# Performance work log

Measured on AMD Instinct MI355X. Metric: run time of the kernel, lower is better.

Reference implementation:

```python
import jax, jax.numpy as jnp
import numpy as np

D_MODEL = 1024
N_HEADS = 16
D_K = D_MODEL // N_HEADS
NEG = -1e10


def setup_inputs() -> dict:
    key = jax.random.key(0)
    ks = jax.random.split(key, 12)
    bs, sl = 2, 2048
    q = jax.random.normal(ks[0], (bs, sl, D_MODEL), dtype=jnp.float32)
    k = jax.random.normal(ks[1], (bs, sl, D_MODEL), dtype=jnp.float32)
    v = jax.random.normal(ks[2], (bs, sl, D_MODEL), dtype=jnp.float32)
    mask = jax.random.randint(ks[3], (bs, 1, sl, sl), 0, 2).astype(bool)
    s = 1.0 / np.sqrt(D_MODEL)
    Wq = jax.random.uniform(ks[4], (D_MODEL, D_MODEL), jnp.float32, -s, s)
    bq = jax.random.uniform(ks[5], (D_MODEL,), jnp.float32, -s, s)
    Wk = jax.random.uniform(ks[6], (D_MODEL, D_MODEL), jnp.float32, -s, s)
    bk = jax.random.uniform(ks[7], (D_MODEL,), jnp.float32, -s, s)
    Wv = jax.random.uniform(ks[8], (D_MODEL, D_MODEL), jnp.float32, -s, s)
    bv = jax.random.uniform(ks[9], (D_MODEL,), jnp.float32, -s, s)
    Wo = jax.random.uniform(ks[10], (D_MODEL, D_MODEL), jnp.float32, -s, s)
    bo = jax.random.uniform(ks[11], (D_MODEL,), jnp.float32, -s, s)
    return {"q": q, "k": k, "v": v, "mask": mask,
            "Wq": Wq, "bq": bq, "Wk": Wk, "bk": bk,
            "Wv": Wv, "bv": bv, "Wo": Wo, "bo": bo}


def reference(q, k, v, mask, Wq, bq, Wk, bk, Wv, bv, Wo, bo):
    bs, sl, _ = q.shape
    sl2 = k.shape[1]
    # linear projections (torch Linear: x @ W.T + b), split into heads: [b, h, s, d_k]
    qh = (q @ Wq.T + bq).reshape(bs, sl, N_HEADS, D_K).transpose(0, 2, 1, 3)
    kh = (k @ Wk.T + bk).reshape(bs, sl2, N_HEADS, D_K).transpose(0, 2, 1, 3)
    vh = (v @ Wv.T + bv).reshape(bs, sl2, N_HEADS, D_K).transpose(0, 2, 1, 3)
    scores = jnp.einsum('bhqd,bhkd->bhqk', qh, kh) / jnp.sqrt(jnp.float32(D_K))
    scores = jnp.where(mask, NEG, scores)
    attn = jax.nn.softmax(scores, axis=-1)
    z = jnp.einsum('bhqk,bhkd->bhqd', attn, vh)  # [b, h, sl, d_k]
    z = z.transpose(0, 2, 1, 3).reshape(bs, sl, D_MODEL)
    return z @ Wo.T + bo
```

## Files before the change

### kernel.cpp

```cpp
#include <hip/hip_runtime.h>

typedef __attribute__((ext_vector_type(8))) short short8;
typedef __attribute__((ext_vector_type(4))) float f32x4;
typedef __attribute__((ext_vector_type(16))) float f32x16;
typedef __attribute__((ext_vector_type(4))) unsigned int u32x4;

#define MFMA16(a, b, c) __builtin_amdgcn_mfma_f32_16x16x32_bf16((a), (b), (c), 0, 0, 0)
#define MFMA32(a, b, c) __builtin_amdgcn_mfma_f32_32x32x16_bf16((a), (b), (c), 0, 0, 0)

#if __has_builtin(__builtin_amdgcn_exp2f)
#define EXP2(x) __builtin_amdgcn_exp2f(x)
#else
#define EXP2(x) __expf((x) * 0.6931471805599453f)
#endif

__device__ __forceinline__ unsigned short f2bf(float f) {
  unsigned int u = __float_as_uint(f);
  u += 0x7FFFu + ((u >> 16) & 1u);
  return (unsigned short)(u >> 16);
}

__device__ __forceinline__ unsigned int cvtpk(float lo, float hi) {
  unsigned int r;
  asm("v_cvt_pk_bf16_f32 %0, %1, %2" : "=v"(r) : "v"(lo), "v"(hi));
  return r;
}

__device__ __forceinline__ short8 mk8(unsigned int a, unsigned int b,
                                      unsigned int c, unsigned int d) {
  u32x4 u = {a, b, c, d};
  return __builtin_bit_cast(short8, u);
}

__device__ __forceinline__ void gload16(const void* g, void* l) {
  __builtin_amdgcn_global_load_lds((const __attribute__((address_space(1))) void*)g,
                                   (__attribute__((address_space(3))) void*)l, 16, 0, 0);
}

__device__ __forceinline__ int swz(int row) {
  return (row & 7) ^ (((row >> 3) & 3) << 1);
}

__device__ __forceinline__ short8 fragld64(const unsigned short* base, int row, int kchunk) {
  int cc = kchunk ^ swz(row);
  return *(const short8*)(base + row * 64 + cc * 8);
}

__global__ void cvt3(const float* __restrict__ a, const float* __restrict__ b,
                     const float* __restrict__ c, unsigned short* __restrict__ out, int n4) {
  const float* src = (blockIdx.z == 0) ? a : ((blockIdx.z == 1) ? b : c);
  int i = blockIdx.x * blockDim.x + threadIdx.x;
  if (i >= n4) return;
  float4 v = ((const float4*)src)[i];
  ushort4 o;
  o.x = f2bf(v.x); o.y = f2bf(v.y); o.z = f2bf(v.z); o.w = f2bf(v.w);
  ((ushort4*)(out + (size_t)blockIdx.z * (size_t)n4 * 4))[i] = o;
}

__global__ void cvt4(const float* __restrict__ a, const float* __restrict__ b,
                     const float* __restrict__ c, const float* __restrict__ d,
                     unsigned short* __restrict__ out, int n4) {
  const float* src = (blockIdx.z == 0) ? a : ((blockIdx.z == 1) ? b
                   : ((blockIdx.z == 2) ? c : d));
  int i = blockIdx.x * blockDim.x + threadIdx.x;
  if (i >= n4) return;
  float4 v = ((const float4*)src)[i];
  ushort4 o;
  o.x = f2bf(v.x); o.y = f2bf(v.y); o.z = f2bf(v.z); o.w = f2bf(v.w);
  ((ushort4*)(out + (size_t)blockIdx.z * (size_t)n4 * 4))[i] = o;
}

__global__ void maskpack(const int* __restrict__ m, unsigned long long* __restrict__ mw) {
  const int lane = threadIdx.x & 63;
  const size_t wbase = ((size_t)blockIdx.x * (blockDim.x >> 6) + (threadIdx.x >> 6)) * 4ull;
#pragma unroll
  for (int u = 0; u < 4; ++u) {
    size_t word = wbase + u;
    int x = m[word * 64 + lane];
    unsigned long long bb = __ballot(x != 0);
    if (lane == 0) mw[word] = bb;
  }
}

__global__ void vtrans(const unsigned short* __restrict__ vh, unsigned short* __restrict__ vtg) {
  __shared__ unsigned short t[64][66];
  const int sx = blockIdx.x * 64, h = blockIdx.y, b = blockIdx.z;
  const int tid = threadIdx.x;
  const int r = tid >> 2, c0 = (tid & 3) * 16;
  const unsigned short* src = vh + ((size_t)(b * 2048 + sx + r)) * 1024 + h * 64 + c0;
  short8 x0 = *(const short8*)src;
  short8 x1 = *(const short8*)(src + 8);
#pragma unroll
  for (int e = 0; e < 8; ++e) {
    t[c0 + e][r] = (unsigned short)x0[e];
    t[c0 + 8 + e][r] = (unsigned short)x1[e];
  }
  __syncthreads();
  short8 y0, y1;
#pragma unroll
  for (int e = 0; e < 8; ++e) {
    y0[e] = (short)t[r][c0 + e];
    y1[e] = (short)t[r][c0 + 8 + e];
  }
  unsigned short* dst = vtg + ((size_t)((b * 16 + h) * 64 + r)) * 2048 + sx + c0;
  *(short8*)dst = y0;
  *(short8*)(dst + 8) = y1;
}

template<bool OUT_BF16>
__global__ __launch_bounds__(256, 3) void gemm_bt(
    const unsigned short* __restrict__ Abase, const unsigned short* __restrict__ Bbase,
    const float* __restrict__ bias0, const float* __restrict__ bias1,
    const float* __restrict__ bias2, void* __restrict__ outv, float scale0)
{
  constexpr int K = 1024, N = 1024;
  const int z = blockIdx.z;
  const unsigned short* A = Abase + (size_t)z * 4194304ull;
  const unsigned short* B = Bbase + (size_t)z * 1048576ull;
  const float* bias = (z == 0) ? bias0 : ((z == 1) ? bias1 : bias2);
  const float scale = (z == 0) ? scale0 : 1.0f;

  __shared__ unsigned short ldsA[128 * 64];
  __shared__ unsigned short ldsB[128 * 64];

  const int tid = threadIdx.x;
  const int lane = tid & 63, wid = tid >> 6;
  const int c16 = lane & 15, g = lane >> 4;
  const int m0 = blockIdx.y * 128, n0 = blockIdx.x * 128;
  const int wr = (wid >> 1) * 64, wc = (wid & 1) * 64;

  f32x4 acc[4][4] = {};

  for (int kt = 0; kt < K; kt += 64) {
    __syncthreads();
#pragma unroll
    for (int i = 0; i < 4; ++i) {
      int row = i * 32 + (tid >> 3);
      int cc = tid & 7;
      int scc = cc ^ swz(row);
      gload16(A + (size_t)(m0 + row) * K + kt + scc * 8, ldsA + row * 64 + cc * 8);
      gload16(B + (size_t)(n0 + row) * K + kt + scc * 8, ldsB + row * 64 + cc * 8);
    }
    __syncthreads();
#pragma unroll
    for (int kc = 0; kc < 2; ++kc) {
      short8 af[4], bf[4];
#pragma unroll
      for (int mi = 0; mi < 4; ++mi) af[mi] = fragld64(ldsA, wr + mi * 16 + c16, kc * 4 + g);
#pragma unroll
      for (int ni = 0; ni < 4; ++ni) bf[ni] = fragld64(ldsB, wc + ni * 16 + c16, kc * 4 + g);
#pragma unroll
      for (int mi = 0; mi < 4; ++mi)
#pragma unroll
        for (int ni = 0; ni < 4; ++ni)
          acc[mi][ni] = MFMA16(af[mi], bf[ni], acc[mi][ni]);
    }
  }

#pragma unroll
  for (int mi = 0; mi < 4; ++mi)
#pragma unroll
    for (int ni = 0; ni < 4; ++ni) {
      int col = n0 + wc + ni * 16 + c16;
      float bb = bias[col];
#pragma unroll
      for (int r = 0; r < 4; ++r) {
        int row = m0 + wr + mi * 16 + g * 4 + r;
        float v = (acc[mi][ni][r] + bb) * scale;
        if constexpr (OUT_BF16)
          ((unsigned short*)outv)[(size_t)z * 4194304ull + (size_t)row * N + col] = f2bf(v);
        else
          ((float*)outv)[(size_t)row * N + col] = v;
      }
    }
}

__device__ __forceinline__ void half_step(
    const unsigned short* __restrict__ kb, const unsigned short* __restrict__ vb,
    const short8 qf[4], unsigned int nb, int ql, int hd, int rowoff, int gm0,
    f32x16& z0, f32x16& z1, float& rs_out)
{
  f32x16 s;
#pragma unroll
  for (int m = 0; m < 4; ++m) {
    unsigned int nib = (nb >> (m * 8)) & 0xFu;
#pragma unroll
    for (int c = 0; c < 4; ++c)
      s[m * 4 + c] = ((nib >> c) & 1u) ? -1e10f : 0.0f;
  }
  __builtin_amdgcn_s_setprio(1);
#pragma unroll
  for (int kc = 0; kc < 4; ++kc)
    s = MFMA32(fragld64(kb, rowoff + ql, kc * 2 + hd), qf[kc], s);
  __builtin_amdgcn_s_setprio(0);
#pragma unroll
  for (int i = 0; i < 16; ++i) s[i] = EXP2(s[i]);
  {
    float a0 = (s[0] + s[1]) + (s[2] + s[3]);
    float a1 = (s[4] + s[5]) + (s[6] + s[7]);
    float a2 = (s[8] + s[9]) + (s[10] + s[11]);
    float a3 = (s[12] + s[13]) + (s[14] + s[15]);
    rs_out = (a0 + a1) + (a2 + a3);
  }
  unsigned int wv[8];
#pragma unroll
  for (int i = 0; i < 8; ++i) wv[i] = cvtpk(s[2 * i], s[2 * i + 1]);
  asm("v_permlane32_swap_b32 %0, %1" : "+v"(wv[0]), "+v"(wv[2]));
  asm("v_permlane32_swap_b32 %0, %1" : "+v"(wv[1]), "+v"(wv[3]));
  asm("v_permlane32_swap_b32 %0, %1" : "+v"(wv[4]), "+v"(wv[6]));
  asm("v_permlane32_swap_b32 %0, %1" : "+v"(wv[5]), "+v"(wv[7]));
  __builtin_amdgcn_s_setprio(1);
  {
    short8 pf0 = mk8(wv[0], wv[1], wv[2], wv[3]);
    z0 = MFMA32(pf0, fragld64(vb, ql, gm0 * 2 + hd), z0);
    z1 = MFMA32(pf0, fragld64(vb, 32 + ql, gm0 * 2 + hd), z1);
    short8 pf1 = mk8(wv[4], wv[5], wv[6], wv[7]);
    z0 = MFMA32(pf1, fragld64(vb, ql, (gm0 + 1) * 2 + hd), z0);
    z1 = MFMA32(pf1, fragld64(vb, 32 + ql, (gm0 + 1) * 2 + hd), z1);
  }
  __builtin_amdgcn_s_setprio(0);
}

__global__ __launch_bounds__(256, 3) void attn(
    const unsigned short* __restrict__ qh, const unsigned short* __restrict__ kh,
    const unsigned short* __restrict__ vtg, const unsigned long long* __restrict__ mw,
    unsigned short* __restrict__ zbf)
{
  constexpr int SL = 2048, DM = 1024, NT = SL / 64;
  const int bid = blockIdx.x;
  const int g = bid & 31;
  const int qt = bid >> 5;
  const int h = g & 15, b = g >> 4;

  const int tid = threadIdx.x, lane = tid & 63, w = tid >> 6;
  const int ql = lane & 31, hd = lane >> 5;
  const int qa = qt * 128 + w * 32;

  __shared__ unsigned short kbuf[2][4096];
  __shared__ unsigned short vbuf[2][4096];

  short8 qf[4];
  {
    const size_t qrow = ((size_t)b * SL + qa + ql) * DM + (size_t)h * 64 + hd * 8;
#pragma unroll
    for (int kc = 0; kc < 4; ++kc)
      qf[kc] = *(const short8*)(qh + qrow + kc * 16);
  }

  f32x16 zacc0 = {}, zacc1 = {};
  float lrun = 0.f;

  const unsigned long long* mwq = mw + ((size_t)b * SL + qa + ql) * (SL / 64);
  unsigned long long mwc = mwq[0];

  const int kr = tid >> 3, cc = tid & 7;
  const int r0 = kr, r1 = kr + 32;
  const size_t kbase = (size_t)b * SL * DM + (size_t)h * 64;
  const size_t vbase = (size_t)((b * 16 + h) * 64) * (size_t)SL;
  const unsigned short* kp0 = kh + kbase + (size_t)r0 * DM + (cc ^ swz(r0)) * 8;
  const unsigned short* kp1 = kh + kbase + (size_t)r1 * DM + (cc ^ swz(r1)) * 8;
  const unsigned short* vp0 = vtg + vbase + (size_t)r0 * SL + (cc ^ swz(r0)) * 8;
  const unsigned short* vp1 = vtg + vbase + (size_t)r1 * SL + (cc ^ swz(r1)) * 8;

  gload16(kp0, kbuf[0] + r0 * 64 + cc * 8);
  gload16(kp1, kbuf[0] + r1 * 64 + cc * 8);
  gload16(vp0, vbuf[0] + r0 * 64 + cc * 8);
  gload16(vp1, vbuf[0] + r1 * 64 + cc * 8);

  for (int t = 0; t < NT; ++t) {
    const int cur = t & 1, nxt = cur ^ 1;
    __syncthreads();

    const bool more = (t + 1 < NT);
    unsigned long long mwn = 0;
    if (more) {
      kp0 += 64 * DM; kp1 += 64 * DM; vp0 += 64; vp1 += 64;
      gload16(kp0, kbuf[nxt] + r0 * 64 + cc * 8);
      gload16(kp1, kbuf[nxt] + r1 * 64 + cc * 8);
      gload16(vp0, vbuf[nxt] + r0 * 64 + cc * 8);
      gload16(vp1, vbuf[nxt] + r1 * 64 + cc * 8);
      mwn = mwq[t + 1];
    }

    float rsA, rsB;
    half_step(kbuf[cur], vbuf[cur], qf, ((unsigned int)mwc) >> (hd * 4),
              ql, hd, 0, 0, zacc0, zacc1, rsA);
    half_step(kbuf[cur], vbuf[cur], qf, ((unsigned int)(mwc >> 32)) >> (hd * 4),
              ql, hd, 32, 2, zacc0, zacc1, rsB);
    lrun += rsA + rsB;
    mwc = mwn;
  }

  lrun += __shfl_xor(lrun, 32);

  float invl = (lrun > 0.f) ? 1.f / lrun : 0.f;
#pragma unroll
  for (int reg = 0; reg < 16; ++reg) {
    int qrow = (reg & 3) + 8 * (reg >> 2) + 4 * hd;
    float il = __shfl(invl, qrow);
    size_t orow = ((size_t)b * SL + qa + qrow) * DM + (size_t)h * 64;
    zbf[orow + ql] = f2bf(zacc0[reg] * il);
    zbf[orow + 32 + ql] = f2bf(zacc1[reg] * il);
  }
}

extern "C" void kernel_launch(void* const* d_in, const int* in_sizes, int n_in,
                              void* d_out, int out_size, void* d_ws, size_t ws_size,
                              hipStream_t stream) {
  const float* q  = (const float*)d_in[0];
  const float* k  = (const float*)d_in[1];
  const float* v  = (const float*)d_in[2];
  const int* mask = (const int*)d_in[3];
  const float* Wq = (const float*)d_in[4];
  const float* bq = (const float*)d_in[5];
  const float* Wk = (const float*)d_in[6];
  const float* bk = (const float*)d_in[7];
  const float* Wv = (const float*)d_in[8];
  const float* bv = (const float*)d_in[9];
  const float* Wo = (const float*)d_in[10];
  const float* bo = (const float*)d_in[11];

  char* ws = (char*)d_ws;
  unsigned short* xbf = (unsigned short*)ws;
  unsigned long long* mwb = (unsigned long long*)ws;
  unsigned short* zbf = (unsigned short*)(ws + 2097152);
  unsigned short* wbf = (unsigned short*)(ws + 25165824);
  unsigned short* qkv = (unsigned short*)(ws + 33554432);
  unsigned short* vtg = (unsigned short*)(ws + 58720256);

  cvt3<<<dim3(4096, 1, 3), 256, 0, stream>>>(q, k, v, xbf, 1048576);
  cvt4<<<dim3(1024, 1, 4), 256, 0, stream>>>(Wq, Wk, Wv, Wo, wbf, 262144);

  gemm_bt<true><<<dim3(8, 32, 3), 256, 0, stream>>>(xbf, wbf, bq, bk, bv, (void*)qkv,
                                                    0.125f * 1.44269504088896f);
  maskpack<<<8192, 256, 0, stream>>>(mask, mwb);
  vtrans<<<dim3(32, 16, 2), 256, 0, stream>>>(qkv + 8388608ull, vtg);
  attn<<<512, 256, 0, stream>>>(qkv, qkv + 4194304ull, vtg, mwb, zbf);
  gemm_bt<false><<<dim3(8, 32, 1), 256, 0, stream>>>(zbf, wbf + 3145728ull, bo, bo, bo, d_out, 1.0f);
}
```

Baseline: 148.0 us.

## Merge prep kernels and double attention K/V tile depth per barrier

The two fp32-to-bf16 conversion kernels become one launch, and the mask packing and V transpose kernels become another, cutting the launch count from seven to five. The attention loop now loads two 64-key tiles per stage, giving a 128-key stage, so there are half as many __syncthreads per row block and more loads in flight. LDS use per block doubles to 64KB, which may cut occupancy below the 3 blocks per CU set by launch bounds.

Result: no change. 147.1 us (-0.6%).

```diff
diff --git a/kernel.cpp b/kernel.cpp
--- a/kernel.cpp
+++ b/kernel.cpp
@@ -46,46 +46,50 @@
   return *(const short8*)(base + row * 64 + cc * 8);
 }
 
-__global__ void cvt3(const float* __restrict__ a, const float* __restrict__ b,
-                     const float* __restrict__ c, unsigned short* __restrict__ out, int n4) {
-  const float* src = (blockIdx.z == 0) ? a : ((blockIdx.z == 1) ? b : c);
-  int i = blockIdx.x * blockDim.x + threadIdx.x;
-  if (i >= n4) return;
-  float4 v = ((const float4*)src)[i];
+__global__ void prep(const float* __restrict__ q, const float* __restrict__ k,
+                     const float* __restrict__ v, const float* __restrict__ Wq,
+                     const float* __restrict__ Wk, const float* __restrict__ Wv,
+                     const float* __restrict__ Wo, unsigned short* __restrict__ xbf,
+                     unsigned short* __restrict__ wbf) {
+  const int bid = blockIdx.x, tid = threadIdx.x;
+  const float* src;
+  unsigned short* dst;
+  int i;
+  if (bid < 12288) {
+    int which = bid >> 12;
+    i = (bid & 4095) * 256 + tid;
+    src = (which == 0) ? q : ((which == 1) ? k : v);
+    dst = xbf + (size_t)which * 4194304ull;
+  } else {
+    int which = (bid - 12288) >> 10;
+    i = ((bid - 12288) & 1023) * 256 + tid;
+    src = (which == 0) ? Wq : ((which == 1) ? Wk : ((which == 2) ? Wv : Wo));
+    dst = wbf + (size_t)which * 1048576ull;
+  }
+  float4 vv = ((const float4*)src)[i];
   ushort4 o;
-  o.x = f2bf(v.x); o.y = f2bf(v.y); o.z = f2bf(v.z); o.w = f2bf(v.w);
-  ((ushort4*)(out + (size_t)blockIdx.z * (size_t)n4 * 4))[i] = o;
-}
-
-__global__ void cvt4(const float* __restrict__ a, const float* __restrict__ b,
-                     const float* __restrict__ c, const float* __restrict__ d,
-                     unsigned short* __restrict__ out, int n4) {
-  const float* src = (blockIdx.z == 0) ? a : ((blockIdx.z == 1) ? b
-                   : ((blockIdx.z == 2) ? c : d));
-  int i = blockIdx.x * blockDim.x + threadIdx.x;
-  if (i >= n4) return;
-  float4 v = ((const float4*)src)[i];
-  ushort4 o;
-  o.x = f2bf(v.x); o.y = f2bf(v.y); o.z = f2bf(v.z); o.w = f2bf(v.w);
-  ((ushort4*)(out + (size_t)blockIdx.z * (size_t)n4 * 4))[i] = o;
-}
-
-__global__ void maskpack(const int* __restrict__ m, unsigned long long* __restrict__ mw) {
-  const int lane = threadIdx.x & 63;
-  const size_t wbase = ((size_t)blockIdx.x * (blockDim.x >> 6) + (threadIdx.x >> 6)) * 4ull;
-#pragma unroll
-  for (int u = 0; u < 4; ++u) {
-    size_t word = wbase + u;
-    int x = m[word * 64 + lane];
-    unsigned long long bb = __ballot(x != 0);
-    if (lane == 0) mw[word] = bb;
-  }
-}
-
-__global__ void vtrans(const unsigned short* __restrict__ vh, unsigned short* __restrict__ vtg) {
+  o.x = f2bf(vv.x); o.y = f2bf(vv.y); o.z = f2bf(vv.z); o.w = f2bf(vv.w);
+  ((ushort4*)dst)[i] = o;
+}
+
+__global__ void post(const int* __restrict__ m, unsigned long long* __restrict__ mw,
+                     const unsigned short* __restrict__ vh, unsigned short* __restrict__ vtg) {
   __shared__ unsigned short t[64][66];
-  const int sx = blockIdx.x * 64, h = blockIdx.y, b = blockIdx.z;
-  const int tid = threadIdx.x;
+  const int bid = blockIdx.x, tid = threadIdx.x;
+  if (bid < 8192) {
+    const int lane = tid & 63;
+    const size_t wbase = ((size_t)bid * 4 + (tid >> 6)) * 4ull;
+#pragma unroll
+    for (int u = 0; u < 4; ++u) {
+      size_t word = wbase + u;
+      int x = m[word * 64 + lane];
+      unsigned long long bb = __ballot(x != 0);
+      if (lane == 0) mw[word] = bb;
+    }
+    return;
+  }
+  const int idx = bid - 8192;
+  const int sx = (idx & 31) * 64, h = (idx >> 5) & 15, b = idx >> 9;
   const int r = tid >> 2, c0 = (tid & 3) * 16;
   const unsigned short* src = vh + ((size_t)(b * 2048 + sx + r)) * 1024 + h * 64 + c0;
   short8 x0 = *(const short8*)src;
@@ -226,7 +230,7 @@
     const unsigned short* __restrict__ vtg, const unsigned long long* __restrict__ mw,
     unsigned short* __restrict__ zbf)
 {
-  constexpr int SL = 2048, DM = 1024, NT = SL / 64;
+  constexpr int SL = 2048, DM = 1024, NSTEP = SL / 128;
   const int bid = blockIdx.x;
   const int g = bid & 31;
   const int qt = bid >> 5;
@@ -236,8 +240,8 @@
   const int ql = lane & 31, hd = lane >> 5;
   const int qa = qt * 128 + w * 32;
 
-  __shared__ unsigned short kbuf[2][4096];
-  __shared__ unsigned short vbuf[2][4096];
+  __shared__ unsigned short kbuf[2][2][4096];
+  __shared__ unsigned short vbuf[2][2][4096];
 
   short8 qf[4];
   {
@@ -251,7 +255,7 @@
   float lrun = 0.f;
 
   const unsigned long long* mwq = mw + ((size_t)b * SL + qa + ql) * (SL / 64);
-  unsigned long long mwc = mwq[0];
+  unsigned long long mwc0 = mwq[0], mwc1 = mwq[1];
 
   const int kr = tid >> 3, cc = tid & 7;
   const int r0 = kr, r1 = kr + 32;
@@ -262,33 +266,47 @@
   const unsigned short* vp0 = vtg + vbase + (size_t)r0 * SL + (cc ^ swz(r0)) * 8;
   const unsigned short* vp1 = vtg + vbase + (size_t)r1 * SL + (cc ^ swz(r1)) * 8;
 
-  gload16(kp0, kbuf[0] + r0 * 64 + cc * 8);
-  gload16(kp1, kbuf[0] + r1 * 64 + cc * 8);
-  gload16(vp0, vbuf[0] + r0 * 64 + cc * 8);
-  gload16(vp1, vbuf[0] + r1 * 64 + cc * 8);
-
-  for (int t = 0; t < NT; ++t) {
-    const int cur = t & 1, nxt = cur ^ 1;
+  gload16(kp0, kbuf[0][0] + r0 * 64 + cc * 8);
+  gload16(kp1, kbuf[0][0] + r1 * 64 + cc * 8);
+  gload16(kp0 + 64 * DM, kbuf[0][1] + r0 * 64 + cc * 8);
+  gload16(kp1 + 64 * DM, kbuf[0][1] + r1 * 64 + cc * 8);
+  gload16(vp0, vbuf[0][0] + r0 * 64 + cc * 8);
+  gload16(vp1, vbuf[0][0] + r1 * 64 + cc * 8);
+  gload16(vp0 + 64, vbuf[0][1] + r0 * 64 + cc * 8);
+  gload16(vp1 + 64, vbuf[0][1] + r1 * 64 + cc * 8);
+
+  for (int st = 0; st < NSTEP; ++st) {
+    const int cur = st & 1, nxt = cur ^ 1;
     __syncthreads();
 
-    const bool more = (t + 1 < NT);
-    unsigned long long mwn = 0;
+    const bool more = (st + 1 < NSTEP);
+    unsigned long long mwn0 = 0, mwn1 = 0;
     if (more) {
-      kp0 += 64 * DM; kp1 += 64 * DM; vp0 += 64; vp1 += 64;
-      gload16(kp0, kbuf[nxt] + r0 * 64 + cc * 8);
-      gload16(kp1, kbuf[nxt] + r1 * 64 + cc * 8);
-      gload16(vp0, vbuf[nxt] + r0 * 64 + cc * 8);
-      gload16(vp1, vbuf[nxt] + r1 * 64 + cc * 8);
-      mwn = mwq[t + 1];
-    }
-
-    float rsA, rsB;
-    half_step(kbuf[cur], vbuf[cur], qf, ((unsigned int)mwc) >> (hd * 4),
-              ql, hd, 0, 0, zacc0, zacc1, rsA);
-    half_step(kbuf[cur], vbuf[cur], qf, ((unsigned int)(mwc >> 32)) >> (hd * 4),
-              ql, hd, 32, 2, zacc0, zacc1, rsB);
-    lrun += rsA + rsB;
-    mwc = mwn;
+      kp0 += 128 * DM; kp1 += 128 * DM; vp0 += 128; vp1 += 128;
+      gload16(kp0, kbuf[nxt][0] + r0 * 64 + cc * 8);
+      gload16(kp1, kbuf[nxt][0] + r1 * 64 + cc * 8);
+      gload16(kp0 + 64 * DM, kbuf[nxt][1] + r0 * 64 + cc * 8);
+      gload16(kp1 + 64 * DM, kbuf[nxt][1] + r1 * 64 + cc * 8);
+      gload16(vp0, vbuf[nxt][0] + r0 * 64 + cc * 8);
+      gload16(vp1, vbuf[nxt][0] + r1 * 64 + cc * 8);
+      gload16(vp0 + 64, vbuf[nxt][1] + r0 * 64 + cc * 8);
+      gload16(vp1 + 64, vbuf[nxt][1] + r1 * 64 + cc * 8);
+      mwn0 = mwq[2 * st + 2];
+      mwn1 = mwq[2 * st + 3];
+    }
+
+    float rs0, rs1, rs2, rs3;
+    half_step(kbuf[cur][0], vbuf[cur][0], qf, ((unsigned int)mwc0) >> (hd * 4),
+              ql, hd, 0, 0, zacc0, zacc1, rs0);
+    half_step(kbuf[cur][0], vbuf[cur][0], qf, ((unsigned int)(mwc0 >> 32)) >> (hd * 4),
+              ql, hd, 32, 2, zacc0, zacc1, rs1);
+    half_step(kbuf[cur][1], vbuf[cur][1], qf, ((unsigned int)mwc1) >> (hd * 4),
+              ql, hd, 0, 0, zacc0, zacc1, rs2);
+    half_step(kbuf[cur][1], vbuf[cur][1], qf, ((unsigned int)(mwc1 >> 32)) >> (hd * 4),
+              ql, hd, 32, 2, zacc0, zacc1, rs3);
+    lrun += (rs0 + rs1) + (rs2 + rs3);
+    mwc0 = mwn0;
+    mwc1 = mwn1;
   }
 
   lrun += __shfl_xor(lrun, 32);
@@ -328,13 +346,11 @@
   unsigned short* qkv = (unsigned short*)(ws + 33554432);
   unsigned short* vtg = (unsigned short*)(ws + 58720256);
 
-  cvt3<<<dim3(4096, 1, 3), 256, 0, stream>>>(q, k, v, xbf, 1048576);
-  cvt4<<<dim3(1024, 1, 4), 256, 0, stream>>>(Wq, Wk, Wv, Wo, wbf, 262144);
+  prep<<<16384, 256, 0, stream>>>(q, k, v, Wq, Wk, Wv, Wo, xbf, wbf);
 
   gemm_bt<true><<<dim3(8, 32, 3), 256, 0, stream>>>(xbf, wbf, bq, bk, bv, (void*)qkv,
                                                     0.125f * 1.44269504088896f);
-  maskpack<<<8192, 256, 0, stream>>>(mask, mwb);
-  vtrans<<<dim3(32, 16, 2), 256, 0, stream>>>(qkv + 8388608ull, vtg);
+  post<<<9216, 256, 0, stream>>>(mask, mwb, qkv + 8388608ull, vtg);
   attn<<<512, 256, 0, stream>>>(qkv, qkv + 4194304ull, vtg, mwb, zbf);
   gemm_bt<false><<<dim3(8, 32, 1), 256, 0, stream>>>(zbf, wbf + 3145728ull, bo, bo, bo, d_out, 1.0f);
 }
```
